# Kernel tuning notes

Hardware: AMD Instinct MI355X
Metric: run time of the kernel (lower is better)

Reference implementation:

```python
import jax, jax.numpy as jnp
import numpy as np

NEG_SLOPE = 0.01  # torch.nn.LeakyReLU default


def setup_inputs() -> dict:
    key = jax.random.key(0)
    ks = jax.random.split(key, 9)
    N_W, N_I, E = 100000, 100000, 2000000
    C_IN, C_OUT, N_CLS = 256, 64, 10
    sc_in = 1.0 / np.sqrt(C_IN)
    sc_cat = 1.0 / np.sqrt(2 * C_OUT)
    return {
        "x_worker": jax.random.normal(ks[0], (N_W, C_IN), dtype=jnp.float32),
        "x_item": jax.random.normal(ks[1], (N_I, C_IN), dtype=jnp.float32),
        "edge_index": jax.random.randint(ks[2], (2, E), 0, N_W, dtype=jnp.int32),
        "W_worker": jax.random.uniform(ks[3], (C_IN, C_OUT), jnp.float32, -sc_in, sc_in),
        "b_worker": jax.random.uniform(ks[4], (C_OUT,), jnp.float32, -sc_in, sc_in),
        "W_item": jax.random.uniform(ks[5], (C_IN, C_OUT), jnp.float32, -sc_in, sc_in),
        "b_item": jax.random.uniform(ks[6], (C_OUT,), jnp.float32, -sc_in, sc_in),
        "W_edge": jax.random.uniform(ks[7], (2 * C_OUT, N_CLS), jnp.float32, -sc_cat, sc_cat),
        "b_edge": jax.random.uniform(ks[8], (N_CLS,), jnp.float32, -sc_cat, sc_cat),
    }


def reference(x_worker, x_item, edge_index, W_worker, b_worker, W_item, b_item, W_edge, b_edge):
    # encoders: Linear + LeakyReLU  -> [N, C_OUT]
    xw = jax.nn.leaky_relu(x_worker @ W_worker + b_worker, NEG_SLOPE)
    xi = jax.nn.leaky_relu(x_item @ W_item + b_item, NEG_SLOPE)
    # gather endpoints per edge and concat -> [E, 2*C_OUT]
    x_cat = jnp.concatenate([xw[edge_index[0]], xi[edge_index[1]]], axis=-1)
    logits = x_cat @ W_edge + b_edge  # [E, num_class]
    return xw, xi, jax.nn.log_softmax(logits, axis=-1)
```

## Files before the change

### kernel.cpp

```cpp
#include <hip/hip_runtime.h>
#include <hip/hip_bf16.h>

#define LOG2E 1.4426950408889634f
#define LN2   0.6931471805599453f

typedef __attribute__((ext_vector_type(8))) short bf16x8;
typedef __attribute__((ext_vector_type(4))) float f32x4;

static __device__ __forceinline__ short f2bf(float f) {
  __hip_bfloat16 h = __float2bfloat16(f);
  return *reinterpret_cast<short*>(&h);
}

static __device__ __forceinline__ void gll16(const float* gsrc, float* ldst) {
  __builtin_amdgcn_global_load_lds(
      (const __attribute__((address_space(1))) void*)gsrc,
      (__attribute__((address_space(3))) void*)ldst, 16, 0, 0);
}

__global__ __launch_bounds__(256) void wprep_kernel(
    const float* __restrict__ Ww, const float* __restrict__ Wi,
    ushort* __restrict__ wfrag)
{
  int id = blockIdx.x * 256 + threadIdx.x;
  if (id >= 4096) return;
  int enc  = id >> 11;
  int f    = (id >> 6) & 31;
  int l    = id & 63;
  int nsub = f >> 3, ks = f & 7;
  const float* __restrict__ W = enc ? Wi : Ww;
  int n  = nsub * 16 + (l & 15);
  int k0 = ks * 32 + (l >> 4) * 8;
  ushort* dst = wfrag + ((size_t)(enc * 32 + f) * 64 + l) * 8;
#pragma unroll
  for (int j = 0; j < 8; ++j)
    dst[j] = (ushort)f2bf(W[(size_t)(k0 + j) * 64 + n]);
}

__global__ __launch_bounds__(256, 3) void enc_mfma6_kernel(
    const float* __restrict__ x0, const float* __restrict__ b0,
    const float* __restrict__ x1, const float* __restrict__ b1,
    const ushort* __restrict__ wfrag, float* __restrict__ out, int M)
{
  __shared__ float xtile[3][4096];

  const int enc = blockIdx.y;
  const float* __restrict__ x   = enc ? x1 : x0;
  const float* __restrict__ bia = enc ? b1 : b0;
  float* __restrict__ o = out + (size_t)enc * (size_t)M * 64u;

  const int lane = threadIdx.x & 63;
  const int wid  = threadIdx.x >> 6;
  const int rsel = lane & 15;
  const int kgrp = lane >> 4;
  const int sw   = rsel & 7;

  const int nstrips = M >> 4;
  const int bx = blockIdx.x, G = gridDim.x;
  const int niter = (bx < nstrips) ? ((nstrips - 1 - bx) / G + 1) : 0;
  if (niter == 0) return;

  bf16x8 wf[8];
#pragma unroll
  for (int ks = 0; ks < 8; ++ks) {
    wf[ks] = *(const bf16x8*)(wfrag +
        ((size_t)((enc * 32 + wid * 8 + ks) * 64 + lane)) * 8);
    asm volatile("" : "+v"(wf[ks]));
  }
  float bv = bia[wid * 16 + rsel];
  asm volatile("" : "+v"(bv));

  auto stage = [&](int s, int buf) {
#pragma unroll
    for (int j = 0; j < 4; ++j) {
      int R = wid * 4 + j;
      const float* gs = x + (size_t)(s * 16 + R) * 256u + ((lane ^ (R & 7)) << 2);
      gll16(gs, &xtile[buf][R * 256]);
    }
  };

  stage(bx, 0);
  stage(bx + ((1 < niter) ? 1 : (niter - 1)) * G, 1);
  stage(bx + ((2 < niter) ? 2 : (niter - 1)) * G, 2);
  __builtin_amdgcn_sched_barrier(0);

  for (int k = 0; k < niter; ++k) {
    if (k == 0)      asm volatile("s_waitcnt vmcnt(8)" ::: "memory");
    else if (k == 1) asm volatile("s_waitcnt vmcnt(12)" ::: "memory");
    else             asm volatile("s_waitcnt vmcnt(16)" ::: "memory");
    __builtin_amdgcn_sched_barrier(0);
    __builtin_amdgcn_s_barrier();
    __builtin_amdgcn_sched_barrier(0);

    const int b = k % 3;
    unsigned base = (unsigned)(unsigned long)
        (__attribute__((address_space(3))) char*)&xtile[b][0];
    unsigned rowb = base + (unsigned)(rsel << 10);

    f32x4 rv[16];
#pragma unroll
    for (int ks = 0; ks < 8; ++ks) {
      int c0 = ks * 8 + kgrp * 2;
      unsigned a0 = rowb + (unsigned)(((c0)     ^ sw) << 4);
      unsigned a1 = rowb + (unsigned)(((c0 + 1) ^ sw) << 4);
      asm volatile("ds_read_b128 %0, %1" : "=&v"(rv[2 * ks])     : "v"(a0));
      asm volatile("ds_read_b128 %0, %1" : "=&v"(rv[2 * ks + 1]) : "v"(a1));
    }
    asm volatile("s_waitcnt lgkmcnt(0)" ::: "memory");
    __builtin_amdgcn_sched_barrier(0);
    __builtin_amdgcn_s_barrier();
    __builtin_amdgcn_sched_barrier(0);

    int sn = k + 3; if (sn >= niter) sn = niter - 1;
    stage(bx + sn * G, b);
    __builtin_amdgcn_sched_barrier(0);

    bf16x8 a[8];
#pragma unroll
    for (int ks = 0; ks < 8; ++ks) {
      f32x4 lo = rv[2 * ks], hi = rv[2 * ks + 1];
      a[ks][0] = f2bf(lo.x); a[ks][1] = f2bf(lo.y);
      a[ks][2] = f2bf(lo.z); a[ks][3] = f2bf(lo.w);
      a[ks][4] = f2bf(hi.x); a[ks][5] = f2bf(hi.y);
      a[ks][6] = f2bf(hi.z); a[ks][7] = f2bf(hi.w);
    }

    f32x4 acc = f32x4{0.f, 0.f, 0.f, 0.f};
#pragma unroll
    for (int ks = 0; ks < 8; ++ks)
      acc = __builtin_amdgcn_mfma_f32_16x16x32_bf16(a[ks], wf[ks], acc, 0, 0, 0);

    const int s = bx + k * G;
    const int crow = s * 16 + kgrp * 4;
    float* orow = o + (size_t)crow * 64u + wid * 16 + rsel;
#pragma unroll
    for (int r = 0; r < 4; ++r) {
      float v = acc[r] + bv;
      v = fmaxf(v, 0.01f * v);
      orow[r * 64] = v;
    }
    __builtin_amdgcn_sched_barrier(0);
  }
}

__global__ __launch_bounds__(256) void proj_kernel(
    const float* __restrict__ feats, const float* __restrict__ W_edge,
    const float* __restrict__ b_edge, float* __restrict__ ws, int M)
{
  const int enc = blockIdx.y;
  int row = blockIdx.x * 256 + threadIdx.x;
  if (row >= M) return;
  const float4* __restrict__ f4 =
      (const float4*)(feats + ((size_t)enc * M + row) * 64u);
  const float* __restrict__ W2 = W_edge + enc * 640;

  float acc[10];
#pragma unroll
  for (int k = 0; k < 10; ++k) acc[k] = enc ? 0.f : b_edge[k];

#pragma unroll 4
  for (int n4 = 0; n4 < 16; ++n4) {
    float4 xv = f4[n4];
    const float* w = W2 + n4 * 40;
#pragma unroll
    for (int k = 0; k < 10; ++k) acc[k] = fmaf(xv.x, w[k],      acc[k]);
#pragma unroll
    for (int k = 0; k < 10; ++k) acc[k] = fmaf(xv.y, w[10 + k], acc[k]);
#pragma unroll
    for (int k = 0; k < 10; ++k) acc[k] = fmaf(xv.z, w[20 + k], acc[k]);
#pragma unroll
    for (int k = 0; k < 10; ++k) acc[k] = fmaf(xv.w, w[30 + k], acc[k]);
  }

  float* orow = ws + ((size_t)enc * M + row) * 16u;
#pragma unroll
  for (int k = 0; k < 10; ++k) orow[k] = acc[k];
}

__global__ __launch_bounds__(256) void edge_kernel(
    const int* __restrict__ ei, const float* __restrict__ ws,
    float* __restrict__ out, int E, int M)
{
  __shared__ float sm[2560];
  long e = (long)blockIdx.x * 256 + threadIdx.x;
  float l[10];
#pragma unroll
  for (int k = 0; k < 10; ++k) l[k] = 0.f;

  if (e < E) {
    int e0 = ei[e];
    int e1 = ei[E + e];
    const float4* pw = (const float4*)ws + (size_t)e0 * 4u;
    const float4* pi = (const float4*)ws + ((size_t)M + e1) * 4u;
    float4 a0 = pw[0], a1 = pw[1], a2 = pw[2];
    float4 c0 = pi[0], c1 = pi[1], c2 = pi[2];
    l[0] = a0.x + c0.x; l[1] = a0.y + c0.y; l[2] = a0.z + c0.z; l[3] = a0.w + c0.w;
    l[4] = a1.x + c1.x; l[5] = a1.y + c1.y; l[6] = a1.z + c1.z; l[7] = a1.w + c1.w;
    l[8] = a2.x + c2.x; l[9] = a2.y + c2.y;
    float m = l[0];
#pragma unroll
    for (int k = 1; k < 10; ++k) m = fmaxf(m, l[k]);
    float s = 0.f;
#pragma unroll
    for (int k = 0; k < 10; ++k) { l[k] = (l[k] - m) * LOG2E; s += exp2f(l[k]); }
    float ls = log2f(s);
#pragma unroll
    for (int k = 0; k < 10; ++k) l[k] = (l[k] - ls) * LN2;
  }

#pragma unroll
  for (int k = 0; k < 10; ++k) sm[threadIdx.x * 10 + k] = l[k];
  __syncthreads();
  const f32x4* sm4 = (const f32x4*)sm;
  f32x4* ob = (f32x4*)(out + (size_t)blockIdx.x * 2560u);
  long lim4 = ((long)E * 10) >> 2;
  long base4 = (long)blockIdx.x * 640;
#pragma unroll
  for (int j = 0; j < 3; ++j) {
    int idx = j * 256 + threadIdx.x;
    if (idx < 640 && base4 + idx < lim4) ob[idx] = sm4[idx];
  }
}

__global__ __launch_bounds__(256) void enc_kernel_f32(
    const float* __restrict__ x0, const float* __restrict__ W0, const float* __restrict__ b0,
    const float* __restrict__ x1, const float* __restrict__ W1, const float* __restrict__ b1,
    float* __restrict__ out, int M)
{
  const int enc = blockIdx.y;
  const float* __restrict__ x = enc ? x1 : x0;
  const float* __restrict__ W = enc ? W1 : W0;
  const float* __restrict__ b = enc ? b1 : b0;
  float* __restrict__ o = out + (size_t)enc * (size_t)M * 64u;

  const int lane = threadIdx.x & 63;
  const int wid  = threadIdx.x >> 6;
  int row0 = __builtin_amdgcn_readfirstlane(blockIdx.x * 64 + wid * 16);
  const float* __restrict__ xrow = x + (size_t)row0 * 256u;

  float acc[16];
#pragma unroll
  for (int r = 0; r < 16; ++r) acc[r] = 0.f;

  if (row0 + 16 <= M) {
#pragma unroll 4
    for (int k = 0; k < 256; ++k) {
      float wv = W[k * 64 + lane];
#pragma unroll
      for (int r = 0; r < 16; ++r)
        acc[r] = fmaf(xrow[r * 256 + k], wv, acc[r]);
    }
    float bias = b[lane];
#pragma unroll
    for (int r = 0; r < 16; ++r) {
      float v = acc[r] + bias;
      v = fmaxf(v, 0.01f * v);
      o[(size_t)(row0 + r) * 64u + lane] = v;
    }
  } else if (row0 < M) {
    int nr = M - row0;
    for (int k = 0; k < 256; ++k) {
      float wv = W[k * 64 + lane];
      for (int r = 0; r < nr; ++r)
        acc[r] = fmaf(xrow[r * 256 + k], wv, acc[r]);
    }
    float bias = b[lane];
    for (int r = 0; r < nr; ++r) {
      float v = acc[r] + bias;
      v = fmaxf(v, 0.01f * v);
      o[(size_t)(row0 + r) * 64u + lane] = v;
    }
  }
}

__global__ __launch_bounds__(256) void edge_kernel_direct(
    const int* __restrict__ ei, const float* __restrict__ feats,
    const float* __restrict__ W_edge, const float* __restrict__ b_edge,
    float* __restrict__ out, int E, int M)
{
  __shared__ float sm[2560];
  long e = (long)blockIdx.x * 256 + threadIdx.x;
  float l[10];
#pragma unroll
  for (int k = 0; k < 10; ++k) l[k] = 0.f;

  if (e < E) {
    int e0 = ei[e];
    int e1 = ei[E + e];
#pragma unroll
    for (int k = 0; k < 10; ++k) l[k] = b_edge[k];
    const float4* fw = (const float4*)(feats + (size_t)e0 * 64u);
    const float4* fi = (const float4*)(feats + ((size_t)M + e1) * 64u);
#pragma unroll 4
    for (int n4 = 0; n4 < 16; ++n4) {
      float4 xv = fw[n4];
      const float* w = W_edge + n4 * 40;
#pragma unroll
      for (int k = 0; k < 10; ++k) l[k] = fmaf(xv.x, w[k],      l[k]);
#pragma unroll
      for (int k = 0; k < 10; ++k) l[k] = fmaf(xv.y, w[10 + k], l[k]);
#pragma unroll
      for (int k = 0; k < 10; ++k) l[k] = fmaf(xv.z, w[20 + k], l[k]);
#pragma unroll
      for (int k = 0; k < 10; ++k) l[k] = fmaf(xv.w, w[30 + k], l[k]);
    }
#pragma unroll 4
    for (int n4 = 0; n4 < 16; ++n4) {
      float4 xv = fi[n4];
      const float* w = W_edge + 640 + n4 * 40;
#pragma unroll
      for (int k = 0; k < 10; ++k) l[k] = fmaf(xv.x, w[k],      l[k]);
#pragma unroll
      for (int k = 0; k < 10; ++k) l[k] = fmaf(xv.y, w[10 + k], l[k]);
#pragma unroll
      for (int k = 0; k < 10; ++k) l[k] = fmaf(xv.z, w[20 + k], l[k]);
#pragma unroll
      for (int k = 0; k < 10; ++k) l[k] = fmaf(xv.w, w[30 + k], l[k]);
    }
    float m = l[0];
#pragma unroll
    for (int k = 1; k < 10; ++k) m = fmaxf(m, l[k]);
    float s = 0.f;
#pragma unroll
    for (int k = 0; k < 10; ++k) { l[k] = (l[k] - m) * LOG2E; s += exp2f(l[k]); }
    float ls = log2f(s);
#pragma unroll
    for (int k = 0; k < 10; ++k) l[k] = (l[k] - ls) * LN2;
  }

#pragma unroll
  for (int k = 0; k < 10; ++k) sm[threadIdx.x * 10 + k] = l[k];
  __syncthreads();
  const f32x4* sm4 = (const f32x4*)sm;
  f32x4* ob = (f32x4*)(out + (size_t)blockIdx.x * 2560u);
  long lim4 = ((long)E * 10) >> 2;
  long base4 = (long)blockIdx.x * 640;
#pragma unroll
  for (int j = 0; j < 3; ++j) {
    int idx = j * 256 + threadIdx.x;
    if (idx < 640 && base4 + idx < lim4) ob[idx] = sm4[idx];
  }
}

extern "C" void kernel_launch(void* const* d_in, const int* in_sizes, int n_in,
                              void* d_out, int out_size, void* d_ws, size_t ws_size,
                              hipStream_t stream)
{
  const float* x_w = (const float*)d_in[0];
  const float* x_i = (const float*)d_in[1];
  const int*   ei  = (const int*)d_in[2];
  const float* W_w = (const float*)d_in[3];
  const float* b_w = (const float*)d_in[4];
  const float* W_i = (const float*)d_in[5];
  const float* b_i = (const float*)d_in[6];
  const float* W_e = (const float*)d_in[7];
  const float* b_e = (const float*)d_in[8];
  float* out = (float*)d_out;

  const int M = in_sizes[0] / 256;
  const int E = in_sizes[2] / 2;

  float* logout = out + (size_t)2 * (size_t)M * 64u;

  const size_t pw_bytes = (size_t)2 * (size_t)M * 16u * sizeof(float);
  const size_t ws_need  = pw_bytes + 65536;

  if (ws_size >= ws_need && (M % 16) == 0) {
    float*  ws    = (float*)d_ws;
    ushort* wfrag = (ushort*)((char*)d_ws + pw_bytes);

    wprep_kernel<<<16, 256, 0, stream>>>(W_w, W_i, wfrag);

    dim3 gA(384, 2);
    enc_mfma6_kernel<<<gA, 256, 0, stream>>>(x_w, b_w, x_i, b_i, wfrag, out, M);

    dim3 gB((M + 255) / 256, 2);
    proj_kernel<<<gB, 256, 0, stream>>>(out, W_e, b_e, ws, M);

    dim3 gC((unsigned)((E + 255) / 256));
    edge_kernel<<<gC, 256, 0, stream>>>(ei, ws, logout, E, M);
  } else {
    dim3 gA0((M + 63) / 64, 2);
    enc_kernel_f32<<<gA0, 256, 0, stream>>>(x_w, W_w, b_w, x_i, W_i, b_i, out, M);
    dim3 gC((unsigned)((E + 255) / 256));
    edge_kernel_direct<<<gC, 256, 0, stream>>>(ei, out, W_e, b_e, logout, E, M);
  }
}
```

Baseline: 142.6 us.

## Replace persistent triple-buffered encoder with one-strip-per-block simple kernel

The persistent encoder used a 384-block grid with triple-buffered async global-to-LDS loads and manual waitcnt/barrier scheduling. It is replaced by a plain kernel that launches one block per 16-row strip, copies the strip into swizzled LDS with ordinary vector loads, and runs the MFMA chain once. This drops the hand-tuned pipeline and its fixed grid in favour of many short blocks, relying on hardware occupancy to hide latency. The trade is more launch and setup overhead per strip, since the weight fragments are reloaded in every block, and no explicit overlap of loads with compute inside a block.

```diff
diff --git a/kernel.cpp b/kernel.cpp
--- a/kernel.cpp
+++ b/kernel.cpp
@@ -10,12 +10,6 @@
 static __device__ __forceinline__ short f2bf(float f) {
   __hip_bfloat16 h = __float2bfloat16(f);
   return *reinterpret_cast<short*>(&h);
-}
-
-static __device__ __forceinline__ void gll16(const float* gsrc, float* ldst) {
-  __builtin_amdgcn_global_load_lds(
-      (const __attribute__((address_space(1))) void*)gsrc,
-      (__attribute__((address_space(3))) void*)ldst, 16, 0, 0);
 }
 
 __global__ __launch_bounds__(256) void wprep_kernel(
@@ -37,109 +31,61 @@
     dst[j] = (ushort)f2bf(W[(size_t)(k0 + j) * 64 + n]);
 }
 
-__global__ __launch_bounds__(256, 3) void enc_mfma6_kernel(
+__global__ __launch_bounds__(256) void enc_simple_kernel(
     const float* __restrict__ x0, const float* __restrict__ b0,
     const float* __restrict__ x1, const float* __restrict__ b1,
     const ushort* __restrict__ wfrag, float* __restrict__ out, int M)
 {
-  __shared__ float xtile[3][4096];
+  __shared__ f32x4 xt[1024];
 
   const int enc = blockIdx.y;
   const float* __restrict__ x   = enc ? x1 : x0;
   const float* __restrict__ bia = enc ? b1 : b0;
   float* __restrict__ o = out + (size_t)enc * (size_t)M * 64u;
 
-  const int lane = threadIdx.x & 63;
-  const int wid  = threadIdx.x >> 6;
+  const int t    = threadIdx.x;
+  const int lane = t & 63;
+  const int wid  = t >> 6;
   const int rsel = lane & 15;
   const int kgrp = lane >> 4;
   const int sw   = rsel & 7;
-
-  const int nstrips = M >> 4;
-  const int bx = blockIdx.x, G = gridDim.x;
-  const int niter = (bx < nstrips) ? ((nstrips - 1 - bx) / G + 1) : 0;
-  if (niter == 0) return;
+  const int strip = blockIdx.x;
 
   bf16x8 wf[8];
 #pragma unroll
-  for (int ks = 0; ks < 8; ++ks) {
+  for (int ks = 0; ks < 8; ++ks)
     wf[ks] = *(const bf16x8*)(wfrag +
         ((size_t)((enc * 32 + wid * 8 + ks) * 64 + lane)) * 8);
-    asm volatile("" : "+v"(wf[ks]));
-  }
   float bv = bia[wid * 16 + rsel];
-  asm volatile("" : "+v"(bv));
-
-  auto stage = [&](int s, int buf) {
-#pragma unroll
-    for (int j = 0; j < 4; ++j) {
-      int R = wid * 4 + j;
-      const float* gs = x + (size_t)(s * 16 + R) * 256u + ((lane ^ (R & 7)) << 2);
-      gll16(gs, &xtile[buf][R * 256]);
-    }
-  };
-
-  stage(bx, 0);
-  stage(bx + ((1 < niter) ? 1 : (niter - 1)) * G, 1);
-  stage(bx + ((2 < niter) ? 2 : (niter - 1)) * G, 2);
-  __builtin_amdgcn_sched_barrier(0);
-
-  for (int k = 0; k < niter; ++k) {
-    if (k == 0)      asm volatile("s_waitcnt vmcnt(8)" ::: "memory");
-    else if (k == 1) asm volatile("s_waitcnt vmcnt(12)" ::: "memory");
-    else             asm volatile("s_waitcnt vmcnt(16)" ::: "memory");
-    __builtin_amdgcn_sched_barrier(0);
-    __builtin_amdgcn_s_barrier();
-    __builtin_amdgcn_sched_barrier(0);
-
-    const int b = k % 3;
-    unsigned base = (unsigned)(unsigned long)
-        (__attribute__((address_space(3))) char*)&xtile[b][0];
-    unsigned rowb = base + (unsigned)(rsel << 10);
-
-    f32x4 rv[16];
-#pragma unroll
-    for (int ks = 0; ks < 8; ++ks) {
-      int c0 = ks * 8 + kgrp * 2;
-      unsigned a0 = rowb + (unsigned)(((c0)     ^ sw) << 4);
-      unsigned a1 = rowb + (unsigned)(((c0 + 1) ^ sw) << 4);
-      asm volatile("ds_read_b128 %0, %1" : "=&v"(rv[2 * ks])     : "v"(a0));
-      asm volatile("ds_read_b128 %0, %1" : "=&v"(rv[2 * ks + 1]) : "v"(a1));
-    }
-    asm volatile("s_waitcnt lgkmcnt(0)" ::: "memory");
-    __builtin_amdgcn_sched_barrier(0);
-    __builtin_amdgcn_s_barrier();
-    __builtin_amdgcn_sched_barrier(0);
-
-    int sn = k + 3; if (sn >= niter) sn = niter - 1;
-    stage(bx + sn * G, b);
-    __builtin_amdgcn_sched_barrier(0);
-
-    bf16x8 a[8];
-#pragma unroll
-    for (int ks = 0; ks < 8; ++ks) {
-      f32x4 lo = rv[2 * ks], hi = rv[2 * ks + 1];
-      a[ks][0] = f2bf(lo.x); a[ks][1] = f2bf(lo.y);
-      a[ks][2] = f2bf(lo.z); a[ks][3] = f2bf(lo.w);
-      a[ks][4] = f2bf(hi.x); a[ks][5] = f2bf(hi.y);
-      a[ks][6] = f2bf(hi.z); a[ks][7] = f2bf(hi.w);
-    }
-
-    f32x4 acc = f32x4{0.f, 0.f, 0.f, 0.f};
-#pragma unroll
-    for (int ks = 0; ks < 8; ++ks)
-      acc = __builtin_amdgcn_mfma_f32_16x16x32_bf16(a[ks], wf[ks], acc, 0, 0, 0);
-
-    const int s = bx + k * G;
-    const int crow = s * 16 + kgrp * 4;
-    float* orow = o + (size_t)crow * 64u + wid * 16 + rsel;
-#pragma unroll
-    for (int r = 0; r < 4; ++r) {
-      float v = acc[r] + bv;
-      v = fmaxf(v, 0.01f * v);
-      orow[r * 64] = v;
-    }
-    __builtin_amdgcn_sched_barrier(0);
+
+  const f32x4* __restrict__ xs = (const f32x4*)(x + (size_t)strip * 4096u);
+#pragma unroll
+  for (int p = 0; p < 4; ++p) {
+    int idx = p * 256 + t;
+    int row = idx >> 6, ch = idx & 63;
+    xt[row * 64 + (ch ^ (row & 7))] = xs[idx];
+  }
+  __syncthreads();
+
+  f32x4 acc = f32x4{0.f, 0.f, 0.f, 0.f};
+#pragma unroll
+  for (int ks = 0; ks < 8; ++ks) {
+    int c0 = ks * 8 + kgrp * 2;
+    f32x4 lo = xt[rsel * 64 + ((c0    ) ^ sw)];
+    f32x4 hi = xt[rsel * 64 + ((c0 + 1) ^ sw)];
+    bf16x8 a;
+    a[0] = f2bf(lo.x); a[1] = f2bf(lo.y); a[2] = f2bf(lo.z); a[3] = f2bf(lo.w);
+    a[4] = f2bf(hi.x); a[5] = f2bf(hi.y); a[6] = f2bf(hi.z); a[7] = f2bf(hi.w);
+    acc = __builtin_amdgcn_mfma_f32_16x16x32_bf16(a, wf[ks], acc, 0, 0, 0);
+  }
+
+  const int crow = strip * 16 + kgrp * 4;
+  float* orow = o + (size_t)crow * 64u + wid * 16 + rsel;
+#pragma unroll
+  for (int r = 0; r < 4; ++r) {
+    float v = acc[r] + bv;
+    v = fmaxf(v, 0.01f * v);
+    orow[r * 64] = v;
   }
 }
 
@@ -371,8 +317,8 @@
 
     wprep_kernel<<<16, 256, 0, stream>>>(W_w, W_i, wfrag);
 
-    dim3 gA(384, 2);
-    enc_mfma6_kernel<<<gA, 256, 0, stream>>>(x_w, b_w, x_i, b_i, wfrag, out, M);
+    dim3 gA((unsigned)(M / 16), 2);
+    enc_simple_kernel<<<gA, 256, 0, stream>>>(x_w, b_w, x_i, b_i, wfrag, out, M);
 
     dim3 gB((M + 255) / 256, 2);
     proj_kernel<<<gB, 256, 0, stream>>>(out, W_e, b_e, ws, M);
```

Result: slower. 148.3 us (+4.1%).
